# Performance work log

Hardware: AMD Instinct MI355X
Metric: run time of the kernel (lower is better)

## Reference

```python
import jax, jax.numpy as jnp
import numpy as np

TEMPERATURE = 0.5
LAMBDA_REG = 0.1
NUM_GROUPS = 4  # number of distinct sensitive-attribute values
EPS = 1e-8      # torch cosine_similarity norm clamp


def setup_inputs() -> dict:
    key = jax.random.key(0)
    k1, k2, k3 = jax.random.split(key, 3)
    B, D = 4096, 256
    return {
        "z_i": jax.random.normal(k1, (B, D), dtype=jnp.float32),
        "z_j": jax.random.normal(k2, (B, D), dtype=jnp.float32),
        "sensitive_features": jax.random.randint(k3, (B,), 0, NUM_GROUPS, dtype=jnp.int64),
    }


def reference(z_i, z_j, sensitive_features):
    B = z_i.shape[0]
    z = jnp.concatenate([z_i, z_j], axis=0)                       # [2B, D]
    norm = jnp.maximum(jnp.linalg.norm(z, axis=1, keepdims=True), EPS)
    zn = z / norm                                                  # row-normalized
    S = zn @ zn.T                                                  # [2B, 2B] cosine sims

    # NT-Xent contrastive term
    pos = jnp.concatenate([jnp.diagonal(S, offset=B), jnp.diagonal(S, offset=-B)])  # [2B]
    mask = 1.0 - jnp.eye(2 * B, dtype=S.dtype)                     # zero out self-sims
    den = jnp.sum(mask * jnp.exp(S / TEMPERATURE), axis=1)         # [2B]
    contrastive = jnp.sum(-(pos / TEMPERATURE) + jnp.log(den)) / (2 * B)

    # Fairness penalty over groups of the FIRST B rows (indices come from sensitive_features)
    Sg = S[:B, :B]
    onehot = jax.nn.one_hot(sensitive_features, NUM_GROUPS, dtype=S.dtype)  # [B, G]
    group_sums = jnp.sum(onehot * (Sg @ onehot), axis=0)           # [G] sum_{i,j in g} S[i,j] (incl. diag, as torch)
    counts = jnp.sum(onehot, axis=0)                               # [G]
    per_group = jnp.where(counts > 1, group_sums / (counts * (counts - 1.0)), 0.0)
    num_unique = jnp.sum(counts > 0).astype(S.dtype)
    fairness = LAMBDA_REG * (jnp.sum(per_group) / num_unique)

    return contrastive + fairness
```

## Files before the change

kernel.cpp:

```cpp
#include <hip/hip_runtime.h>
#include <hip/hip_bf16.h>

typedef __attribute__((ext_vector_type(8))) short short8;
typedef __attribute__((ext_vector_type(4))) float f32x4;
typedef __attribute__((address_space(1))) const void gvoid_t;
typedef __attribute__((address_space(3))) void lvoid_t;

#define NB 4096
#define DD 256
#define TWOB 8192
#define NMACRO 1056u
#define GSUM_BLOCKS 16

__device__ __forceinline__ unsigned short f2bf(float f) {
  unsigned int u = __float_as_uint(f);
  u += 0x7fffu + ((u >> 16) & 1u);
  return (unsigned short)(u >> 16);
}
__device__ __forceinline__ float bf2f(unsigned short s) {
  return __uint_as_float(((unsigned int)s) << 16);
}


__global__ __launch_bounds__(256) void norm_kernel(const float* __restrict__ zi,
                                                   const float* __restrict__ zj,
                                                   float* __restrict__ wsf,
                                                   float* __restrict__ ppos,
                                                   unsigned short* __restrict__ znb) {
  __shared__ float sred[4];
  if (blockIdx.x < 32) wsf[blockIdx.x * 256 + threadIdx.x] = 0.f;
  const int lane = threadIdx.x & 63, wave = threadIdx.x >> 6;
  const int i = blockIdx.x * 4 + wave;

  float4 a = ((const float4*)(zi + (size_t)i * DD))[lane];
  float4 b = ((const float4*)(zj + (size_t)i * DD))[lane];
  float sa = a.x * a.x + a.y * a.y + a.z * a.z + a.w * a.w;
  float sb = b.x * b.x + b.y * b.y + b.z * b.z + b.w * b.w;
  float sab = a.x * b.x + a.y * b.y + a.z * b.z + a.w * b.w;
#pragma unroll
  for (int m = 32; m >= 1; m >>= 1) {
    sa += __shfl_xor(sa, m);
    sb += __shfl_xor(sb, m);
    sab += __shfl_xor(sab, m);
  }
  float ra = 1.0f / fmaxf(sqrtf(sa), 1e-8f);
  float rb = 1.0f / fmaxf(sqrtf(sb), 1e-8f);
  ushort4 oa, ob;
  oa.x = f2bf(a.x * ra); oa.y = f2bf(a.y * ra); oa.z = f2bf(a.z * ra); oa.w = f2bf(a.w * ra);
  ob.x = f2bf(b.x * rb); ob.y = f2bf(b.y * rb); ob.z = f2bf(b.z * rb); ob.w = f2bf(b.w * rb);
  ((ushort4*)(znb + (size_t)i * DD))[lane] = oa;
  ((ushort4*)(znb + (size_t)(i + NB) * DD))[lane] = ob;

  if (lane == 0) sred[wave] = sab * ra * rb;
  __syncthreads();
  if (threadIdx.x == 0)
    ppos[blockIdx.x] = sred[0] + sred[1] + sred[2] + sred[3];
}

__global__ __launch_bounds__(512, 4) void den_kernel(const int* __restrict__ sf,
                                                     float* __restrict__ wsf,
                                                     const unsigned short* __restrict__ znb,
                                                     float* __restrict__ vsum_part,
                                                     int* __restrict__ cnt_part) {
  __shared__ __align__(16) unsigned short As[2][4096];
  __shared__ __align__(16) unsigned short Bs[2][8192];

  float* den = wsf;

  const int tid = threadIdx.x;
  const int lane = tid & 63, wave = tid >> 6;
  const unsigned t_lin = blockIdx.y * 64u + blockIdx.x;

  if (t_lin < GSUM_BLOCKS) {
    const int b = (int)t_lin;
    const int r0 = b * 256;
    float acc[4][4];
#pragma unroll
    for (int q = 0; q < 4; ++q)
#pragma unroll
      for (int e = 0; e < 4; ++e) acc[q][e] = 0.f;
    int cnt[4] = {0, 0, 0, 0};
    const int rw = r0 + wave * 32;
    for (int k = 0; k < 32; ++k) {
      int row = rw + k;
      int g = sf[row];
      ushort4 v = ((const ushort4*)(znb + (size_t)row * DD))[lane];
      float f0 = bf2f(v.x), f1 = bf2f(v.y), f2 = bf2f(v.z), f3 = bf2f(v.w);
#pragma unroll
      for (int q = 0; q < 4; ++q) {
        bool sel = (g == q);
        acc[q][0] += sel ? f0 : 0.f;
        acc[q][1] += sel ? f1 : 0.f;
        acc[q][2] += sel ? f2 : 0.f;
        acc[q][3] += sel ? f3 : 0.f;
        cnt[q] += sel ? 1 : 0;
      }
    }
    float4* lsd = (float4*)&Bs[0][0];
    int* lcnt = (int*)&As[0][0];
#pragma unroll
    for (int q = 0; q < 4; ++q) {
      float4 t;
      t.x = acc[q][0]; t.y = acc[q][1]; t.z = acc[q][2]; t.w = acc[q][3];
      lsd[(wave * 4 + q) * 64 + lane] = t;
    }
    if (lane == 0) {
#pragma unroll
      for (int q = 0; q < 4; ++q) lcnt[wave * 4 + q] = cnt[q];
    }
    __syncthreads();
    if (tid < 256) {
      int g = tid >> 6, l = tid & 63;
      float4 s = {0.f, 0.f, 0.f, 0.f};
#pragma unroll
      for (int w = 0; w < 8; ++w) {
        float4 sv = lsd[(w * 4 + g) * 64 + l];
        s.x += sv.x; s.y += sv.y; s.z += sv.z; s.w += sv.w;
      }
      ((float4*)(vsum_part + (size_t)(b * 4 + g) * 256))[l] = s;
      if (tid < 4) {
        int ci = 0;
#pragma unroll
        for (int w = 0; w < 8; ++w) ci += lcnt[w * 4 + tid];
        cnt_part[b * 4 + tid] = ci;
      }
    }
    return;
  }
  if (t_lin >= NMACRO + GSUM_BLOCKS) return;

  unsigned t = t_lin - GSUM_BLOCKS;
  unsigned tr = 0;
  while (t >= 32u - (tr >> 1)) { t -= 32u - (tr >> 1); ++tr; }
  unsigned c = (tr >> 1) + t;
  const size_t rowbase = (size_t)tr * 128;
  const size_t colbase = (size_t)c * 256;

  const int u = lane >> 3;
  const int cp = (lane & 7) ^ u;
  const int ri = 2 * u + (cp >> 2);
  const int kelem = (cp & 3) * 8;
  const int slot = ((((lane & 1) << 2) | (lane >> 4)) ^ ((lane >> 1) & 7));
  const int fragoff = ((lane & 15) >> 1) * 128 + slot * 16;
  const int wrow = wave & 1;
  const int wcol = wave >> 1;

  const int tch = (int)(2 * c) + (wcol >> 1);
  const float fr = (tch >= (int)tr) ? 1.f : 0.f;
  const float fc = (tch > (int)tr) ? 1.f : 0.f;

  f32x4 zero = {0.f, 0.f, 0.f, 0.f};
  f32x4 acc[4][4];
#pragma unroll
  for (int i = 0; i < 4; ++i)
#pragma unroll
    for (int j = 0; j < 4; ++j) acc[i][j] = zero;

  const unsigned short* gA = znb + (rowbase + wave * 16 + ri) * DD + kelem;
  const unsigned short* gB0 = znb + (colbase + (2 * wave) * 16 + ri) * DD + kelem;
  const unsigned short* gB1 = gB0 + 16 * DD;

  auto stage = [&](int kt, int buf) {
    __builtin_amdgcn_global_load_lds((gvoid_t*)(gA + kt * 32), (lvoid_t*)&As[buf][wave * 512], 16, 0, 0);
    __builtin_amdgcn_global_load_lds((gvoid_t*)(gB0 + kt * 32), (lvoid_t*)&Bs[buf][(2 * wave) * 512], 16, 0, 0);
    __builtin_amdgcn_global_load_lds((gvoid_t*)(gB1 + kt * 32), (lvoid_t*)&Bs[buf][(2 * wave + 1) * 512], 16, 0, 0);
  };

  stage(0, 0);
  __syncthreads();
#pragma unroll
  for (int kt = 0; kt < 8; ++kt) {
    if (kt < 7) stage(kt + 1, (kt + 1) & 1);
    const int buf = kt & 1;
    short8 af[4], bfr[4];
#pragma unroll
    for (int mi = 0; mi < 4; ++mi)
      af[mi] = *(const short8*)((const char*)&As[0][0] + buf * 8192 + (wrow * 4 + mi) * 1024 + fragoff);
#pragma unroll
    for (int ni = 0; ni < 4; ++ni)
      bfr[ni] = *(const short8*)((const char*)&Bs[0][0] + buf * 16384 + (wcol * 4 + ni) * 1024 + fragoff);
#pragma unroll
    for (int mi = 0; mi < 4; ++mi)
#pragma unroll
      for (int ni = 0; ni < 4; ++ni)
        acc[mi][ni] = __builtin_amdgcn_mfma_f32_16x16x32_bf16(af[mi], bfr[ni], acc[mi][ni], 0, 0, 0);
    __syncthreads();
  }

  float rsum[4][4];
  float csum[4];
#pragma unroll
  for (int mi = 0; mi < 4; ++mi)
#pragma unroll
    for (int r = 0; r < 4; ++r) rsum[mi][r] = 0.f;
#pragma unroll
  for (int ni = 0; ni < 4; ++ni) csum[ni] = 0.f;
#pragma unroll
  for (int mi = 0; mi < 4; ++mi)
#pragma unroll
    for (int ni = 0; ni < 4; ++ni)
#pragma unroll
      for (int r = 0; r < 4; ++r) {
        float e = __expf(2.0f * acc[mi][ni][r]);
        rsum[mi][r] += e;
        csum[ni] += e;
      }
#pragma unroll
  for (int m = 1; m < 16; m <<= 1)
#pragma unroll
    for (int mi = 0; mi < 4; ++mi)
#pragma unroll
      for (int r = 0; r < 4; ++r) rsum[mi][r] += __shfl_xor(rsum[mi][r], m);
#pragma unroll
  for (int m = 16; m < 64; m <<= 1)
#pragma unroll
    for (int ni = 0; ni < 4; ++ni) csum[ni] += __shfl_xor(csum[ni], m);

  float* Lr = (float*)&As[0][0];
  float* Lc = Lr + 512;
  if ((lane & 15) == 0) {
    int h = lane >> 4;
#pragma unroll
    for (int mi = 0; mi < 4; ++mi)
#pragma unroll
      for (int r = 0; r < 4; ++r)
        Lr[wcol * 128 + wrow * 64 + mi * 16 + h * 4 + r] = rsum[mi][r] * fr;
  }
  if (lane < 16) {
#pragma unroll
    for (int ni = 0; ni < 4; ++ni)
      Lc[wrow * 256 + wcol * 64 + ni * 16 + lane] = csum[ni] * fc;
  }
  __syncthreads();
  if (tid < 256) {
    float v = Lc[tid] + Lc[256 + tid];
    if (v != 0.f) unsafeAtomicAdd(&den[colbase + tid], v);
  } else if (tid < 384) {
    int r = tid - 256;
    unsafeAtomicAdd(&den[rowbase + r], Lr[r] + Lr[128 + r] + Lr[256 + r] + Lr[384 + r]);
  }
}

__global__ __launch_bounds__(256) void tail_kernel(const float* __restrict__ wsf,
                                                   const float* __restrict__ vsum_part,
                                                   const int* __restrict__ cnt_part,
                                                   const float* __restrict__ ppos,
                                                   float* __restrict__ out) {
  __shared__ float sred[32];
  const float* den = wsf;
  const int tid = threadIdx.x;
  const int lane = tid & 63, wave = tid >> 6;

  const float e2 = __expf(2.0f);
  float ls = 0.f;
  for (int i = tid; i < TWOB; i += 256) ls += __logf(den[i] - e2);
#pragma unroll
  for (int m = 32; m >= 1; m >>= 1) ls += __shfl_xor(ls, m);
  if (lane == 0) sred[wave] = ls;

  float pp = 0.f;
#pragma unroll
  for (int k = 0; k < 4; ++k) pp += ppos[k * 256 + tid];
#pragma unroll
  for (int m = 32; m >= 1; m >>= 1) pp += __shfl_xor(pp, m);
  if (lane == 0) sred[4 + wave] = pp;

  float gp[4];
#pragma unroll
  for (int g = 0; g < 4; ++g) {
    float v = 0.f;
#pragma unroll
    for (int b = 0; b < 16; ++b) v += vsum_part[(size_t)(b * 4 + g) * 256 + tid];
    gp[g] = v * v;
#pragma unroll
    for (int m = 32; m >= 1; m >>= 1) gp[g] += __shfl_xor(gp[g], m);
  }
  if (lane == 0) {
#pragma unroll
    for (int g = 0; g < 4; ++g) sred[8 + wave * 4 + g] = gp[g];
  }
  __syncthreads();
  if (tid == 0) {
    float lsum = sred[0] + sred[1] + sred[2] + sred[3];
    float psum = sred[4] + sred[5] + sred[6] + sred[7];
    float contrastive = (lsum - 4.0f * psum) / (float)TWOB;
    float fsum = 0.f;
    int uniq = 0;
#pragma unroll
    for (int q = 0; q < 4; ++q) {
      int ci = 0;
#pragma unroll
      for (int b = 0; b < 16; ++b) ci += cnt_part[b * 4 + q];
      float gsq = sred[8 + q] + sred[12 + q] + sred[16 + q] + sred[20 + q];
      float c = (float)ci;
      if (ci > 0) uniq++;
      if (ci > 1) fsum += gsq / (c * (c - 1.0f));
    }
    out[0] = contrastive + 0.1f * (fsum / (uniq > 0 ? (float)uniq : 1.0f));
  }
}

extern "C" void kernel_launch(void* const* d_in, const int* in_sizes, int n_in,
                              void* d_out, int out_size, void* d_ws, size_t ws_size,
                              hipStream_t stream) {
  const float* zi = (const float*)d_in[0];
  const float* zj = (const float*)d_in[1];
  const int* sf = (const int*)d_in[2];
  float* out = (float*)d_out;
  char* ws = (char*)d_ws;
  float* wsf = (float*)ws;
  unsigned short* znb = (unsigned short*)(ws + 65536);
  float* vsum_part = (float*)(ws + 4259840);
  int* cnt_part = (int*)(ws + 4276224);
  float* ppos = (float*)(ws + 4276480);

  hipLaunchKernelGGL(norm_kernel, dim3(1024), dim3(256), 0, stream, zi, zj, wsf, ppos, znb);
  hipLaunchKernelGGL(den_kernel, dim3(64, 17), dim3(512), 0, stream,
                     sf, wsf, znb, vsum_part, cnt_part);
  hipLaunchKernelGGL(tail_kernel, dim3(1), dim3(256), 0, stream,
                     wsf, vsum_part, cnt_part, ppos, out);
}
```

Measured before the change: 109.5 us.

## Triple-buffer den_kernel loads, swizzle block order, widen tail kernel to 1024 threads

The main tile loop moves from double to triple buffering. Explicit vmcnt waits and one barrier per k-step replace the two __syncthreads, so global-to-LDS loads run two stages ahead. Block indices are remapped with an 8-way interleave, likely to spread neighbouring tiles across XCDs or caches. The tail reduction uses 1024 threads so each thread handles fewer serial loads. LDS use grows by half, which may reduce occupancy under launch_bounds(512,4).

```diff
diff --git a/kernel.cpp b/kernel.cpp
--- a/kernel.cpp
+++ b/kernel.cpp
@@ -11,6 +11,7 @@
 #define TWOB 8192
 #define NMACRO 1056u
 #define GSUM_BLOCKS 16
+#define NPART 1072u
 
 __device__ __forceinline__ unsigned short f2bf(float f) {
   unsigned int u = __float_as_uint(f);
@@ -62,14 +63,16 @@
                                                      const unsigned short* __restrict__ znb,
                                                      float* __restrict__ vsum_part,
                                                      int* __restrict__ cnt_part) {
-  __shared__ __align__(16) unsigned short As[2][4096];
-  __shared__ __align__(16) unsigned short Bs[2][8192];
+  __shared__ __align__(16) unsigned short As[3][4096];
+  __shared__ __align__(16) unsigned short Bs[3][8192];
 
   float* den = wsf;
 
   const int tid = threadIdx.x;
   const int lane = tid & 63, wave = tid >> 6;
-  const unsigned t_lin = blockIdx.y * 64u + blockIdx.x;
+  const unsigned t_raw = blockIdx.y * 64u + blockIdx.x;
+  if (t_raw >= NPART) return;
+  const unsigned t_lin = (t_raw & 7u) * 134u + (t_raw >> 3);
 
   if (t_lin < GSUM_BLOCKS) {
     const int b = (int)t_lin;
@@ -127,7 +130,6 @@
     }
     return;
   }
-  if (t_lin >= NMACRO + GSUM_BLOCKS) return;
 
   unsigned t = t_lin - GSUM_BLOCKS;
   unsigned tr = 0;
@@ -167,11 +169,15 @@
   };
 
   stage(0, 0);
-  __syncthreads();
+  stage(1, 1);
 #pragma unroll
   for (int kt = 0; kt < 8; ++kt) {
-    if (kt < 7) stage(kt + 1, (kt + 1) & 1);
-    const int buf = kt & 1;
+    const int buf = kt % 3;
+    if (kt < 7) asm volatile("s_waitcnt vmcnt(3)" ::: "memory");
+    else        asm volatile("s_waitcnt vmcnt(0)" ::: "memory");
+    __builtin_amdgcn_s_barrier();
+    asm volatile("" ::: "memory");
+    if (kt < 6) stage(kt + 2, (kt + 2) % 3);
     short8 af[4], bfr[4];
 #pragma unroll
     for (int mi = 0; mi < 4; ++mi)
@@ -184,7 +190,6 @@
 #pragma unroll
       for (int ni = 0; ni < 4; ++ni)
         acc[mi][ni] = __builtin_amdgcn_mfma_f32_16x16x32_bf16(af[mi], bfr[ni], acc[mi][ni], 0, 0, 0);
-    __syncthreads();
   }
 
   float rsum[4][4];
@@ -241,48 +246,44 @@
   }
 }
 
-__global__ __launch_bounds__(256) void tail_kernel(const float* __restrict__ wsf,
-                                                   const float* __restrict__ vsum_part,
-                                                   const int* __restrict__ cnt_part,
-                                                   const float* __restrict__ ppos,
-                                                   float* __restrict__ out) {
-  __shared__ float sred[32];
+__global__ __launch_bounds__(1024) void tail_kernel(const float* __restrict__ wsf,
+                                                    const float* __restrict__ vsum_part,
+                                                    const int* __restrict__ cnt_part,
+                                                    const float* __restrict__ ppos,
+                                                    float* __restrict__ out) {
+  __shared__ float sred[48];
   const float* den = wsf;
   const int tid = threadIdx.x;
   const int lane = tid & 63, wave = tid >> 6;
 
   const float e2 = __expf(2.0f);
   float ls = 0.f;
-  for (int i = tid; i < TWOB; i += 256) ls += __logf(den[i] - e2);
+#pragma unroll
+  for (int k = 0; k < 8; ++k) ls += __logf(den[k * 1024 + tid] - e2);
 #pragma unroll
   for (int m = 32; m >= 1; m >>= 1) ls += __shfl_xor(ls, m);
   if (lane == 0) sred[wave] = ls;
 
-  float pp = 0.f;
-#pragma unroll
-  for (int k = 0; k < 4; ++k) pp += ppos[k * 256 + tid];
+  float pp = ppos[tid];
 #pragma unroll
   for (int m = 32; m >= 1; m >>= 1) pp += __shfl_xor(pp, m);
-  if (lane == 0) sred[4 + wave] = pp;
-
-  float gp[4];
-#pragma unroll
-  for (int g = 0; g < 4; ++g) {
+  if (lane == 0) sred[16 + wave] = pp;
+
+  {
+    int g = tid >> 8, col = tid & 255;
     float v = 0.f;
 #pragma unroll
-    for (int b = 0; b < 16; ++b) v += vsum_part[(size_t)(b * 4 + g) * 256 + tid];
-    gp[g] = v * v;
-#pragma unroll
-    for (int m = 32; m >= 1; m >>= 1) gp[g] += __shfl_xor(gp[g], m);
-  }
-  if (lane == 0) {
-#pragma unroll
-    for (int g = 0; g < 4; ++g) sred[8 + wave * 4 + g] = gp[g];
+    for (int b = 0; b < 16; ++b) v += vsum_part[(size_t)(b * 4 + g) * 256 + col];
+    float gp = v * v;
+#pragma unroll
+    for (int m = 32; m >= 1; m >>= 1) gp += __shfl_xor(gp, m);
+    if (lane == 0) sred[32 + wave] = gp;
   }
   __syncthreads();
   if (tid == 0) {
-    float lsum = sred[0] + sred[1] + sred[2] + sred[3];
-    float psum = sred[4] + sred[5] + sred[6] + sred[7];
+    float lsum = 0.f, psum = 0.f;
+#pragma unroll
+    for (int w = 0; w < 16; ++w) { lsum += sred[w]; psum += sred[16 + w]; }
     float contrastive = (lsum - 4.0f * psum) / (float)TWOB;
     float fsum = 0.f;
     int uniq = 0;
@@ -291,10 +292,10 @@
       int ci = 0;
 #pragma unroll
       for (int b = 0; b < 16; ++b) ci += cnt_part[b * 4 + q];
-      float gsq = sred[8 + q] + sred[12 + q] + sred[16 + q] + sred[20 + q];
-      float c = (float)ci;
+      float gsq = sred[32 + q * 4] + sred[33 + q * 4] + sred[34 + q * 4] + sred[35 + q * 4];
+      float cf = (float)ci;
       if (ci > 0) uniq++;
-      if (ci > 1) fsum += gsq / (c * (c - 1.0f));
+      if (ci > 1) fsum += gsq / (cf * (cf - 1.0f));
     }
     out[0] = contrastive + 0.1f * (fsum / (uniq > 0 ? (float)uniq : 1.0f));
   }
@@ -317,6 +318,6 @@
   hipLaunchKernelGGL(norm_kernel, dim3(1024), dim3(256), 0, stream, zi, zj, wsf, ppos, znb);
   hipLaunchKernelGGL(den_kernel, dim3(64, 17), dim3(512), 0, stream,
                      sf, wsf, znb, vsum_part, cnt_part);
-  hipLaunchKernelGGL(tail_kernel, dim3(1), dim3(256), 0, stream,
+  hipLaunchKernelGGL(tail_kernel, dim3(1), dim3(1024), 0, stream,
                      wsf, vsum_part, cnt_part, ppos, out);
 }
```

Result: faster. 96.65 us (-11.8%).
